# Kernel optimization log

Measured on AMD Instinct MI355X. Metric: run time of the kernel, lower is better.

Reference implementation:

```python
import jax, jax.numpy as jnp
import numpy as np

EMB_DIM = 128
WEIGHT_COL = 24

def setup_inputs() -> dict:
    key = jax.random.key(0)
    ks = jax.random.split(key, 9)
    B, S = 8, 4096
    s_in = 1.0 / np.sqrt(EMB_DIM)
    s_out = 1.0 / np.sqrt(WEIGHT_COL)
    return {
        "x": jax.random.normal(ks[0], (B, S, EMB_DIM), dtype=jnp.float32),
        "wQ": jax.random.uniform(ks[1], (EMB_DIM, WEIGHT_COL), jnp.float32, -s_in, s_in),
        "bQ": jax.random.uniform(ks[2], (WEIGHT_COL,), jnp.float32, -s_in, s_in),
        "wK": jax.random.uniform(ks[3], (EMB_DIM, WEIGHT_COL), jnp.float32, -s_in, s_in),
        "bK": jax.random.uniform(ks[4], (WEIGHT_COL,), jnp.float32, -s_in, s_in),
        "wV": jax.random.uniform(ks[5], (EMB_DIM, WEIGHT_COL), jnp.float32, -s_in, s_in),
        "bV": jax.random.uniform(ks[6], (WEIGHT_COL,), jnp.float32, -s_in, s_in),
        "wO": jax.random.uniform(ks[7], (WEIGHT_COL, EMB_DIM), jnp.float32, -s_out, s_out),
        "bO": jax.random.uniform(ks[8], (EMB_DIM,), jnp.float32, -s_out, s_out),
    }

def reference(x, wQ, bQ, wK, bK, wV, bV, wO, bO):
    # projections: [B,S,E] -> [B,S,D]
    Q = x @ wQ + bQ
    K = x @ wK + bK
    V = x @ wV + bV
    # NOTE: source scales by sqrt(emb_dim), not sqrt(weight_col)
    scale = 1.0 / np.sqrt(EMB_DIM).astype(np.float32)
    scores = jnp.einsum('bqd,bkd->bqk', Q, K) * scale  # [B,S,S]
    A = jax.nn.softmax(scores, axis=-1)
    H = jnp.einsum('bqk,bkd->bqd', A, V)               # [B,S,D]
    return H @ wO + bO                                  # [B,S,E]
```

## Files before the change

### kernel.cpp

```cpp
#include <hip/hip_runtime.h>
#include <hip/hip_fp16.h>


#define B_ 8
#define S_ 4096
#define E_ 128
#define D_ 24
#define N_ (B_ * S_)
#define SCALE 0.08838834764831845f
#define LOG2E 1.4426950408889634f

#define NSP 8
#define KCHUNK (S_ / NSP)

#define HS_STRIDE 40
#define XS_STRIDE 136
#define OS_STRIDE 84

typedef __attribute__((ext_vector_type(8))) short bfrag;
typedef __attribute__((ext_vector_type(4))) float ffrag;

__device__ inline unsigned short f2bf(float f) {
    unsigned int x = __builtin_bit_cast(unsigned int, f);
    return (unsigned short)((x + 0x7fffu + ((x >> 16) & 1u)) >> 16);
}
__device__ inline unsigned int pack2h(float a, float b) {
    unsigned int ua = __builtin_bit_cast(unsigned int, a) + 0x8000u;
    unsigned int ub = __builtin_bit_cast(unsigned int, b) + 0x8000u;
    return __builtin_amdgcn_perm(ub, ua, 0x07060302);
}
__device__ inline unsigned int packh16(float a, float b) {
    return __builtin_bit_cast(unsigned int, __builtin_amdgcn_cvt_pkrtz(a, b));
}

__global__ __launch_bounds__(256) void prep_kernel(
    const float* __restrict__ wQ, const float* __restrict__ bQ,
    const float* __restrict__ wK, const float* __restrict__ bK,
    const float* __restrict__ wV, const float* __restrict__ bV,
    const float* __restrict__ wO,
    unsigned short* __restrict__ Wf, unsigned short* __restrict__ wOf,
    float* __restrict__ bqkv)
{
    const int gtid   = blockIdx.x * 256 + threadIdx.x;
    const int stride = gridDim.x * 256;
    const float qs = SCALE * LOG2E;
    for (int idx = gtid; idx < 4 * 5 * 512; idx += stride) {
        const int j    = idx & 7;
        const int lane = (idx >> 3) & 63;
        const int nt   = (idx >> 9) % 5;
        const int kt   = idx / 2560;
        const int n = nt * 16 + (lane & 15);
        const int k = kt * 32 + ((lane >> 4) << 3) + j;
        float v = 0.0f;
        if (n < 24)      v = wQ[k * 24 + n] * qs;
        else if (n < 48) v = wK[k * 24 + (n - 24)];
        else if (n < 72) v = wV[k * 24 + (n - 48)];
        Wf[idx] = f2bf(v);
    }
    for (int idx = gtid; idx < 8 * 512; idx += stride) {
        const int j    = idx & 7;
        const int lane = (idx >> 3) & 63;
        const int nt   = idx >> 9;
        const int k = ((lane >> 4) << 3) + j;
        const int e = nt * 16 + (lane & 15);
        wOf[idx] = (k < 24) ? f2bf(wO[k * 128 + e]) : (unsigned short)0;
    }
    if (gtid < 80) {
        float v = 0.0f;
        if (gtid < 24)      v = bQ[gtid] * qs;
        else if (gtid < 48) v = bK[gtid - 24];
        else if (gtid < 72) v = bV[gtid - 48];
        bqkv[gtid] = v;
    }
}

__global__ __launch_bounds__(256) void proj_kernel(
    const float* __restrict__ x, const unsigned short* __restrict__ Wf,
    const float* __restrict__ bqkv,
    unsigned short* __restrict__ Qbf, unsigned short* __restrict__ Kbf,
    unsigned short* __restrict__ Vt)
{
    __shared__ float smem[64 * OS_STRIDE];
    unsigned short* xs = (unsigned short*)smem;
    float* os = smem;

    const int tid  = threadIdx.x;
    const int lane = tid & 63;
    const int w    = tid >> 6;
    const int col  = lane & 15;
    const int quad = lane >> 4;
    const int rb   = blockIdx.x * 64;

    #pragma unroll
    for (int i = 0; i < 8; ++i) {
        const int idx = i * 256 + tid;
        const int row = idx >> 5, c4 = idx & 31;
        const float4 xv = *(const float4*)(x + (size_t)(rb + row) * 128 + c4 * 4);
        uint2 h;
        h.x = pack2h(xv.x, xv.y);
        h.y = pack2h(xv.z, xv.w);
        *(uint2*)(&xs[row * XS_STRIDE + c4 * 4]) = h;
    }

    bfrag Wfr[20];
    #pragma unroll
    for (int f = 0; f < 20; ++f)
        Wfr[f] = *(const bfrag*)(Wf + (f * 64 + lane) * 8);

    __syncthreads();

    ffrag acc[5];
    #pragma unroll
    for (int nt = 0; nt < 5; ++nt) acc[nt] = (ffrag){0.f, 0.f, 0.f, 0.f};

    #pragma unroll
    for (int kt = 0; kt < 4; ++kt) {
        const bfrag Af = *(const bfrag*)(&xs[(w * 16 + col) * XS_STRIDE + kt * 32 + quad * 8]);
        #pragma unroll
        for (int nt = 0; nt < 5; ++nt)
            acc[nt] = __builtin_amdgcn_mfma_f32_16x16x32_bf16(Af, Wfr[kt * 5 + nt], acc[nt], 0, 0, 0);
    }

    __syncthreads();

    #pragma unroll
    for (int nt = 0; nt < 5; ++nt) {
        const float bb = bqkv[nt * 16 + col];
        #pragma unroll
        for (int r = 0; r < 4; ++r)
            os[(w * 16 + quad * 4 + r) * OS_STRIDE + nt * 16 + col] = acc[nt][r] + bb;
    }
    __syncthreads();

    {
        const int half  = tid & 1;
        const int row   = (tid >> 1) & 63;
        const int isK   = tid >> 7;
        const int cbase = isK * 24;
        unsigned int pk[8];
        #pragma unroll
        for (int g = 0; g < 8; ++g) {
            const int c0 = half * 16 + g * 2;
            const float f0 = (c0     < 24) ? os[row * OS_STRIDE + cbase + c0]     : 0.0f;
            const float f1 = (c0 + 1 < 24) ? os[row * OS_STRIDE + cbase + c0 + 1] : 0.0f;
            pk[g] = pack2h(f0, f1);
        }
        unsigned short* dst = (isK ? Kbf : Qbf) + (size_t)(rb + row) * 32 + half * 16;
        *(uint4*)(dst)     = make_uint4(pk[0], pk[1], pk[2], pk[3]);
        *(uint4*)(dst + 8) = make_uint4(pk[4], pk[5], pk[6], pk[7]);
    }

    if (tid < 192) {
        const int d  = tid % 24;
        const int ch = tid / 24;
        unsigned int p[4];
        #pragma unroll
        for (int g = 0; g < 4; ++g) {
            const float f0 = os[(ch * 8 + g * 2 + 0) * OS_STRIDE + 48 + d];
            const float f1 = os[(ch * 8 + g * 2 + 1) * OS_STRIDE + 48 + d];
            p[g] = pack2h(f0, f1);
        }
        const int b = rb >> 12, s0 = rb & 4095;
        uint4* dst = (uint4*)(Vt + (((size_t)(b * 32 + d)) << 12) + s0 + ch * 8);
        *dst = make_uint4(p[0], p[1], p[2], p[3]);
    } else if (tid < 200) {
        const int ch = tid - 192;
        const int b = rb >> 12, s0 = rb & 4095;
        uint4* dst = (uint4*)(Vt + (((size_t)(b * 32 + 24)) << 12) + s0 + ch * 8);
        *dst = make_uint4(0x3F803F80u, 0x3F803F80u, 0x3F803F80u, 0x3F803F80u);
    }
}

__global__ __launch_bounds__(256, 6) void attn_kernel(
    const unsigned short* __restrict__ Qbf, const unsigned short* __restrict__ Kbf,
    const unsigned short* __restrict__ Vt,
    __half* __restrict__ Opart, float* __restrict__ lpart)
{
    const int tid    = threadIdx.x;
    const int lane   = tid & 63;
    const int w      = tid >> 6;
    const int col    = lane & 15;
    const int quad   = lane >> 4;
    const int blk    = blockIdx.x;
    const int split  = blockIdx.y;
    const int b      = blk >> 5;
    const int qbase  = blk * 128 + w * 32;

    const bfrag Qf0 = *(const bfrag*)(Qbf + (size_t)(qbase + col) * 32 + quad * 8);
    const bfrag Qf1 = *(const bfrag*)(Qbf + (size_t)(qbase + 16 + col) * 32 + quad * 8);

    const int keyE = ((col >> 2) << 3) + (col & 3);
    const unsigned short* Kp =
        Kbf + ((size_t)b * 4096 + (size_t)split * KCHUNK + keyE) * 32 + quad * 8;
    const int d1 = (16 + col <= 24) ? (16 + col) : 24;
    const unsigned short* Vp0 =
        Vt + ((size_t)(b * 32 + col)) * 4096 + (size_t)split * KCHUNK + quad * 8;
    const unsigned short* Vp1 =
        Vt + ((size_t)(b * 32 + d1)) * 4096 + (size_t)split * KCHUNK + quad * 8;

    ffrag O00 = {0.f,0.f,0.f,0.f};
    ffrag O01 = {0.f,0.f,0.f,0.f};
    ffrag O10 = {0.f,0.f,0.f,0.f};
    ffrag O11 = {0.f,0.f,0.f,0.f};

    bfrag cKfe = *(const bfrag*)(Kp);
    bfrag cKfo = *(const bfrag*)(Kp + 128);
    bfrag cVa0 = *(const bfrag*)(Vp0);
    bfrag cVa1 = *(const bfrag*)(Vp1);

    #pragma unroll
    for (int it = 0; it < KCHUNK; it += 32) {
        bfrag nKfe, nKfo, nVa0, nVa1;
        if (it + 32 < KCHUNK) {
            const unsigned short* Kn  = Kp  + (size_t)(it / 32 + 1) * 1024;
            const unsigned short* Vn0 = Vp0 + (size_t)(it + 32);
            const unsigned short* Vn1 = Vp1 + (size_t)(it + 32);
            nKfe = *(const bfrag*)(Kn);
            nKfo = *(const bfrag*)(Kn + 128);
            nVa0 = *(const bfrag*)(Vn0);
            nVa1 = *(const bfrag*)(Vn1);
        }

        {
            ffrag Se = {0.f,0.f,0.f,0.f}, So = {0.f,0.f,0.f,0.f};
            Se = __builtin_amdgcn_mfma_f32_16x16x32_bf16(cKfe, Qf0, Se, 0, 0, 0);
            So = __builtin_amdgcn_mfma_f32_16x16x32_bf16(cKfo, Qf0, So, 0, 0, 0);
            union { bfrag f; unsigned int u[4]; } P;
            P.u[0] = pack2h(__builtin_amdgcn_exp2f(Se[0]), __builtin_amdgcn_exp2f(Se[1]));
            P.u[1] = pack2h(__builtin_amdgcn_exp2f(Se[2]), __builtin_amdgcn_exp2f(Se[3]));
            P.u[2] = pack2h(__builtin_amdgcn_exp2f(So[0]), __builtin_amdgcn_exp2f(So[1]));
            P.u[3] = pack2h(__builtin_amdgcn_exp2f(So[2]), __builtin_amdgcn_exp2f(So[3]));
            O00 = __builtin_amdgcn_mfma_f32_16x16x32_bf16(cVa0, P.f, O00, 0, 0, 0);
            O01 = __builtin_amdgcn_mfma_f32_16x16x32_bf16(cVa1, P.f, O01, 0, 0, 0);
        }
        {
            ffrag Se = {0.f,0.f,0.f,0.f}, So = {0.f,0.f,0.f,0.f};
            Se = __builtin_amdgcn_mfma_f32_16x16x32_bf16(cKfe, Qf1, Se, 0, 0, 0);
            So = __builtin_amdgcn_mfma_f32_16x16x32_bf16(cKfo, Qf1, So, 0, 0, 0);
            union { bfrag f; unsigned int u[4]; } P;
            P.u[0] = pack2h(__builtin_amdgcn_exp2f(Se[0]), __builtin_amdgcn_exp2f(Se[1]));
            P.u[1] = pack2h(__builtin_amdgcn_exp2f(Se[2]), __builtin_amdgcn_exp2f(Se[3]));
            P.u[2] = pack2h(__builtin_amdgcn_exp2f(So[0]), __builtin_amdgcn_exp2f(So[1]));
            P.u[3] = pack2h(__builtin_amdgcn_exp2f(So[2]), __builtin_amdgcn_exp2f(So[3]));
            O10 = __builtin_amdgcn_mfma_f32_16x16x32_bf16(cVa0, P.f, O10, 0, 0, 0);
            O11 = __builtin_amdgcn_mfma_f32_16x16x32_bf16(cVa1, P.f, O11, 0, 0, 0);
        }

        cKfe = nKfe; cKfo = nKfo; cVa0 = nVa0; cVa1 = nVa1;
    }

    {
        const size_t base0 = ((size_t)split * N_ + qbase + col) * 32;
        uint2 s0;
        s0.x = packh16(O00[0], O00[1]);
        s0.y = packh16(O00[2], O00[3]);
        *(uint2*)(Opart + base0 + quad * 4) = s0;
        if (quad < 2) {
            uint2 s1;
            s1.x = packh16(O01[0], O01[1]);
            s1.y = packh16(O01[2], O01[3]);
            *(uint2*)(Opart + base0 + 16 + quad * 4) = s1;
        }
        if (quad == 2)
            lpart[(size_t)split * N_ + qbase + col] = O01[0];

        const size_t base1 = base0 + 16 * 32;
        uint2 t0;
        t0.x = packh16(O10[0], O10[1]);
        t0.y = packh16(O10[2], O10[3]);
        *(uint2*)(Opart + base1 + quad * 4) = t0;
        if (quad < 2) {
            uint2 t1;
            t1.x = packh16(O11[0], O11[1]);
            t1.y = packh16(O11[2], O11[3]);
            *(uint2*)(Opart + base1 + 16 + quad * 4) = t1;
        }
        if (quad == 2)
            lpart[(size_t)split * N_ + qbase + 16 + col] = O11[0];
    }
}

__global__ __launch_bounds__(256) void combine_kernel(
    const __half* __restrict__ Opart, const float* __restrict__ lpart,
    const unsigned short* __restrict__ wOf, const float* __restrict__ bO,
    float* __restrict__ out)
{
    __shared__ unsigned short Hs[64 * HS_STRIDE];

    const int tid = threadIdx.x;
    const int qb  = blockIdx.x * 64;
    {
        const int ql = tid >> 2;
        const int c8 = (tid & 3) * 8;
        const int q  = qb + ql;
        float a[8] = {0.f, 0.f, 0.f, 0.f, 0.f, 0.f, 0.f, 0.f};
        if (c8 < 24) {
            #pragma unroll
            for (int s = 0; s < NSP; ++s) {
                const __half2* p2 = (const __half2*)(Opart + ((size_t)s * N_ + q) * 32 + c8);
                #pragma unroll
                for (int j = 0; j < 4; ++j) {
                    const float2 f = __half22float2(p2[j]);
                    a[2 * j]     += f.x;
                    a[2 * j + 1] += f.y;
                }
            }
        }
        float ls = 0.f;
        #pragma unroll
        for (int s = 0; s < NSP; ++s) ls += lpart[(size_t)s * N_ + q];
        const float inv = 1.0f / ls;
        uint4 pk;
        pk.x = pack2h(a[0] * inv, a[1] * inv);
        pk.y = pack2h(a[2] * inv, a[3] * inv);
        pk.z = pack2h(a[4] * inv, a[5] * inv);
        pk.w = pack2h(a[6] * inv, a[7] * inv);
        *(uint4*)(&Hs[ql * HS_STRIDE + c8]) = pk;
    }
    __syncthreads();

    const int lane = tid & 63;
    const int w    = tid >> 6;
    const int col  = lane & 15;
    const int quad = lane >> 4;
    const bfrag Hf = *(const bfrag*)(&Hs[(w * 16 + col) * HS_STRIDE + quad * 8]);
    #pragma unroll
    for (int nt = 0; nt < 8; ++nt) {
        const bfrag Wo = *(const bfrag*)(wOf + (nt * 64 + lane) * 8);
        ffrag C = {0.f, 0.f, 0.f, 0.f};
        C = __builtin_amdgcn_mfma_f32_16x16x32_bf16(Hf, Wo, C, 0, 0, 0);
        const float bo = bO[nt * 16 + col];
        #pragma unroll
        for (int r = 0; r < 4; ++r)
            out[(size_t)(qb + w * 16 + quad * 4 + r) * 128 + nt * 16 + col] = C[r] + bo;
    }
}

extern "C" void kernel_launch(void* const* d_in, const int* in_sizes, int n_in,
                              void* d_out, int out_size, void* d_ws, size_t ws_size,
                              hipStream_t stream) {
    const float* x  = (const float*)d_in[0];
    const float* wQ = (const float*)d_in[1];
    const float* bQ = (const float*)d_in[2];
    const float* wK = (const float*)d_in[3];
    const float* bK = (const float*)d_in[4];
    const float* wV = (const float*)d_in[5];
    const float* bV = (const float*)d_in[6];
    const float* wO = (const float*)d_in[7];
    const float* bO = (const float*)d_in[8];
    float* out = (float*)d_out;

    unsigned short* ws16 = (unsigned short*)d_ws;
    unsigned short* Qbf = ws16;
    unsigned short* Kbf = Qbf + (size_t)N_ * 32;
    unsigned short* Vt  = Kbf + (size_t)N_ * 32;
    unsigned short* Wf  = Vt + (size_t)B_ * 32 * S_;
    unsigned short* wOf = Wf + 4 * 5 * 512;
    float* bqkv = (float*)(wOf + 8 * 512);
    __half* Opart = (__half*)(bqkv + 80);
    float* lpart = (float*)(Opart + (size_t)NSP * N_ * 32);

    prep_kernel<<<8, 256, 0, stream>>>(wQ, bQ, wK, bK, wV, bV, wO, Wf, wOf, bqkv);
    proj_kernel<<<N_ / 64, 256, 0, stream>>>(x, Wf, bqkv, Qbf, Kbf, Vt);
    attn_kernel<<<dim3(N_ / 128, NSP), 256, 0, stream>>>(Qbf, Kbf, Vt, Opart, lpart);
    combine_kernel<<<N_ / 64, 256, 0, stream>>>(Opart, lpart, wOf, bO, out);
}
```

Measured before the change: 144.8 us.

## Stage K and V tiles in shared memory for reuse across waves

Instead of each of the four waves loading its own K and V fragments straight from global memory with register double-buffering, the block now cooperatively copies a 128-key tile of K (with the key permutation applied) and the 25 V rows into LDS, synchronizes, then reads the fragments from LDS. This cuts redundant global/L2 traffic by roughly 4x per block. In exchange it adds two barriers per tile, drops the prefetch overlap, and raises the occupancy hint from 6 to 8 waves.

```diff
diff --git a/kernel.cpp b/kernel.cpp
--- a/kernel.cpp
+++ b/kernel.cpp
@@ -12,7 +12,10 @@
 
 #define NSP 8
 #define KCHUNK (S_ / NSP)
-
+#define TK 128
+
+#define KS_STRIDE 40
+#define VS_STRIDE 136
 #define HS_STRIDE 40
 #define XS_STRIDE 136
 #define OS_STRIDE 84
@@ -171,82 +174,91 @@
     }
 }
 
-__global__ __launch_bounds__(256, 6) void attn_kernel(
+__global__ __launch_bounds__(256, 8) void attn_kernel(
     const unsigned short* __restrict__ Qbf, const unsigned short* __restrict__ Kbf,
     const unsigned short* __restrict__ Vt,
     __half* __restrict__ Opart, float* __restrict__ lpart)
 {
-    const int tid    = threadIdx.x;
-    const int lane   = tid & 63;
-    const int w      = tid >> 6;
-    const int col    = lane & 15;
-    const int quad   = lane >> 4;
-    const int blk    = blockIdx.x;
-    const int split  = blockIdx.y;
-    const int b      = blk >> 5;
-    const int qbase  = blk * 128 + w * 32;
+    __shared__ unsigned short Ks[TK * KS_STRIDE];
+    __shared__ unsigned short Vs[25 * VS_STRIDE];
+
+    const int tid   = threadIdx.x;
+    const int lane  = tid & 63;
+    const int w     = tid >> 6;
+    const int col   = lane & 15;
+    const int quad  = lane >> 4;
+    const int blk   = blockIdx.x;
+    const int split = blockIdx.y;
+    const int b     = blk >> 5;
+    const int qbase = blk * 128 + w * 32;
 
     const bfrag Qf0 = *(const bfrag*)(Qbf + (size_t)(qbase + col) * 32 + quad * 8);
     const bfrag Qf1 = *(const bfrag*)(Qbf + (size_t)(qbase + 16 + col) * 32 + quad * 8);
 
-    const int keyE = ((col >> 2) << 3) + (col & 3);
-    const unsigned short* Kp =
-        Kbf + ((size_t)b * 4096 + (size_t)split * KCHUNK + keyE) * 32 + quad * 8;
-    const int d1 = (16 + col <= 24) ? (16 + col) : 24;
-    const unsigned short* Vp0 =
-        Vt + ((size_t)(b * 32 + col)) * 4096 + (size_t)split * KCHUNK + quad * 8;
-    const unsigned short* Vp1 =
-        Vt + ((size_t)(b * 32 + d1)) * 4096 + (size_t)split * KCHUNK + quad * 8;
+    const unsigned short* Kbase = Kbf + ((size_t)b * 4096 + split * KCHUNK) * 32;
+    const unsigned short* Vbase = Vt + (size_t)(b * 32) * 4096 + split * KCHUNK;
+
+    const int r1 = (16 + col <= 24) ? (16 + col) : 24;
 
     ffrag O00 = {0.f,0.f,0.f,0.f};
     ffrag O01 = {0.f,0.f,0.f,0.f};
     ffrag O10 = {0.f,0.f,0.f,0.f};
     ffrag O11 = {0.f,0.f,0.f,0.f};
 
-    bfrag cKfe = *(const bfrag*)(Kp);
-    bfrag cKfo = *(const bfrag*)(Kp + 128);
-    bfrag cVa0 = *(const bfrag*)(Vp0);
-    bfrag cVa1 = *(const bfrag*)(Vp1);
-
-    #pragma unroll
-    for (int it = 0; it < KCHUNK; it += 32) {
-        bfrag nKfe, nKfo, nVa0, nVa1;
-        if (it + 32 < KCHUNK) {
-            const unsigned short* Kn  = Kp  + (size_t)(it / 32 + 1) * 1024;
-            const unsigned short* Vn0 = Vp0 + (size_t)(it + 32);
-            const unsigned short* Vn1 = Vp1 + (size_t)(it + 32);
-            nKfe = *(const bfrag*)(Kn);
-            nKfo = *(const bfrag*)(Kn + 128);
-            nVa0 = *(const bfrag*)(Vn0);
-            nVa1 = *(const bfrag*)(Vn1);
-        }
-
-        {
-            ffrag Se = {0.f,0.f,0.f,0.f}, So = {0.f,0.f,0.f,0.f};
-            Se = __builtin_amdgcn_mfma_f32_16x16x32_bf16(cKfe, Qf0, Se, 0, 0, 0);
-            So = __builtin_amdgcn_mfma_f32_16x16x32_bf16(cKfo, Qf0, So, 0, 0, 0);
-            union { bfrag f; unsigned int u[4]; } P;
-            P.u[0] = pack2h(__builtin_amdgcn_exp2f(Se[0]), __builtin_amdgcn_exp2f(Se[1]));
-            P.u[1] = pack2h(__builtin_amdgcn_exp2f(Se[2]), __builtin_amdgcn_exp2f(Se[3]));
-            P.u[2] = pack2h(__builtin_amdgcn_exp2f(So[0]), __builtin_amdgcn_exp2f(So[1]));
-            P.u[3] = pack2h(__builtin_amdgcn_exp2f(So[2]), __builtin_amdgcn_exp2f(So[3]));
-            O00 = __builtin_amdgcn_mfma_f32_16x16x32_bf16(cVa0, P.f, O00, 0, 0, 0);
-            O01 = __builtin_amdgcn_mfma_f32_16x16x32_bf16(cVa1, P.f, O01, 0, 0, 0);
-        }
-        {
-            ffrag Se = {0.f,0.f,0.f,0.f}, So = {0.f,0.f,0.f,0.f};
-            Se = __builtin_amdgcn_mfma_f32_16x16x32_bf16(cKfe, Qf1, Se, 0, 0, 0);
-            So = __builtin_amdgcn_mfma_f32_16x16x32_bf16(cKfo, Qf1, So, 0, 0, 0);
-            union { bfrag f; unsigned int u[4]; } P;
-            P.u[0] = pack2h(__builtin_amdgcn_exp2f(Se[0]), __builtin_amdgcn_exp2f(Se[1]));
-            P.u[1] = pack2h(__builtin_amdgcn_exp2f(Se[2]), __builtin_amdgcn_exp2f(Se[3]));
-            P.u[2] = pack2h(__builtin_amdgcn_exp2f(So[0]), __builtin_amdgcn_exp2f(So[1]));
-            P.u[3] = pack2h(__builtin_amdgcn_exp2f(So[2]), __builtin_amdgcn_exp2f(So[3]));
-            O10 = __builtin_amdgcn_mfma_f32_16x16x32_bf16(cVa0, P.f, O10, 0, 0, 0);
-            O11 = __builtin_amdgcn_mfma_f32_16x16x32_bf16(cVa1, P.f, O11, 0, 0, 0);
-        }
-
-        cKfe = nKfe; cKfo = nKfo; cVa0 = nVa0; cVa1 = nVa1;
+    for (int kb = 0; kb < KCHUNK; kb += TK) {
+        #pragma unroll
+        for (int i = 0; i < 2; ++i) {
+            const int idx = i * 256 + tid;
+            const int key = idx >> 2, ch = idx & 3;
+            const uint4 t4 = *(const uint4*)(Kbase + (size_t)(kb + key) * 32 + ch * 8);
+            const int row = (key & ~31) + (((key >> 2) & 1) << 4)
+                          + (((key & 31) >> 3) << 2) + (key & 3);
+            *(uint4*)(&Ks[row * KS_STRIDE + ch * 8]) = t4;
+        }
+        #pragma unroll
+        for (int i = 0; i < 2; ++i) {
+            const int idx = i * 256 + tid;
+            if (idx < 400) {
+                const int d = idx >> 4, ch = idx & 15;
+                const uint4 t4 = *(const uint4*)(Vbase + (size_t)d * 4096 + kb + ch * 8);
+                *(uint4*)(&Vs[d * VS_STRIDE + ch * 8]) = t4;
+            }
+        }
+        __syncthreads();
+
+        #pragma unroll
+        for (int c2 = 0; c2 < 4; ++c2) {
+            const bfrag Kfe = *(const bfrag*)(&Ks[(c2 * 32 + col) * KS_STRIDE + quad * 8]);
+            const bfrag Kfo = *(const bfrag*)(&Ks[(c2 * 32 + 16 + col) * KS_STRIDE + quad * 8]);
+            const bfrag Va0 = *(const bfrag*)(&Vs[col * VS_STRIDE + c2 * 32 + quad * 8]);
+            const bfrag Va1 = *(const bfrag*)(&Vs[r1 * VS_STRIDE + c2 * 32 + quad * 8]);
+
+            {
+                ffrag Se = {0.f,0.f,0.f,0.f}, So = {0.f,0.f,0.f,0.f};
+                Se = __builtin_amdgcn_mfma_f32_16x16x32_bf16(Kfe, Qf0, Se, 0, 0, 0);
+                So = __builtin_amdgcn_mfma_f32_16x16x32_bf16(Kfo, Qf0, So, 0, 0, 0);
+                union { bfrag f; unsigned int u[4]; } P;
+                P.u[0] = pack2h(__builtin_amdgcn_exp2f(Se[0]), __builtin_amdgcn_exp2f(Se[1]));
+                P.u[1] = pack2h(__builtin_amdgcn_exp2f(Se[2]), __builtin_amdgcn_exp2f(Se[3]));
+                P.u[2] = pack2h(__builtin_amdgcn_exp2f(So[0]), __builtin_amdgcn_exp2f(So[1]));
+                P.u[3] = pack2h(__builtin_amdgcn_exp2f(So[2]), __builtin_amdgcn_exp2f(So[3]));
+                O00 = __builtin_amdgcn_mfma_f32_16x16x32_bf16(Va0, P.f, O00, 0, 0, 0);
+                O01 = __builtin_amdgcn_mfma_f32_16x16x32_bf16(Va1, P.f, O01, 0, 0, 0);
+            }
+            {
+                ffrag Se = {0.f,0.f,0.f,0.f}, So = {0.f,0.f,0.f,0.f};
+                Se = __builtin_amdgcn_mfma_f32_16x16x32_bf16(Kfe, Qf1, Se, 0, 0, 0);
+                So = __builtin_amdgcn_mfma_f32_16x16x32_bf16(Kfo, Qf1, So, 0, 0, 0);
+                union { bfrag f; unsigned int u[4]; } P;
+                P.u[0] = pack2h(__builtin_amdgcn_exp2f(Se[0]), __builtin_amdgcn_exp2f(Se[1]));
+                P.u[1] = pack2h(__builtin_amdgcn_exp2f(Se[2]), __builtin_amdgcn_exp2f(Se[3]));
+                P.u[2] = pack2h(__builtin_amdgcn_exp2f(So[0]), __builtin_amdgcn_exp2f(So[1]));
+                P.u[3] = pack2h(__builtin_amdgcn_exp2f(So[2]), __builtin_amdgcn_exp2f(So[3]));
+                O10 = __builtin_amdgcn_mfma_f32_16x16x32_bf16(Va0, P.f, O10, 0, 0, 0);
+                O11 = __builtin_amdgcn_mfma_f32_16x16x32_bf16(Va1, P.f, O11, 0, 0, 0);
+            }
+        }
+        __syncthreads();
     }
 
     {
```

New measurement: 125.4 us. 1.15x faster.
